# Performance work log

Hardware: AMD Instinct MI355X
Metric: run time of the kernel (lower is better)

The kernel has to match this reference:

```python
import math
import jax, jax.numpy as jnp
import numpy as np

D_MODEL = 1024
N_HEADS = 16
D_K = D_MODEL // N_HEADS


def setup_inputs() -> dict:
    key = jax.random.key(0)
    ks = jax.random.split(key, 12)
    B, L, D = 8, 2048, D_MODEL
    scale = 1.0 / math.sqrt(D)
    inp = {
        "queries": jax.random.normal(ks[0], (B, L, D), jnp.float32),
        "keys": jax.random.normal(ks[1], (B, L, D), jnp.float32),
        "values": jax.random.normal(ks[2], (B, L, D), jnp.float32),
        "Wq": jax.random.normal(ks[3], (D, D), jnp.float32) * scale,
        "bq": jnp.zeros((D,), jnp.float32),
        "Wk": jax.random.normal(ks[4], (D, D), jnp.float32) * scale,
        "bk": jnp.zeros((D,), jnp.float32),
        "Wv": jax.random.normal(ks[5], (D, D), jnp.float32) * scale,
        "bv": jnp.zeros((D,), jnp.float32),
        "Wo": jax.random.normal(ks[6], (D, D), jnp.float32) * scale,
        "bo": jnp.zeros((D,), jnp.float32),
    }
    return inp


def _autocorr_forward(queries, keys, values, Wq, bq, Wk, bk, Wv, bv, Wo, bo):
    B, L, D = queries.shape
    H, dk = N_HEADS, D_K
    # projections (torch Linear: x @ W.T + b), split heads -> [B, L, H, dk]
    q = (queries @ Wq.T + bq).reshape(B, L, H, dk)
    k = (keys @ Wk.T + bk).reshape(B, L, H, dk)
    v = (values @ Wv.T + bv).reshape(B, L, H, dk)

    # FFT cross-correlation along time, averaged over channel dim: [B, L, H]
    qf = jnp.fft.rfft(q, axis=1)
    kf = jnp.fft.rfft(k, axis=1)
    corr = jnp.fft.irfft(qf * jnp.conj(kf), n=L, axis=1).mean(axis=-1)
    corr = corr.transpose(0, 2, 1)  # [B, H, L]

    topk = min(max(1, int(math.log(L))), L)  # top_k=None default
    weights, delays = jax.lax.top_k(corr, topk)  # [B, H, k]
    w = jax.nn.softmax(weights, axis=-1)

    # modulo-shifted gather indices: [B, H, k, L]
    idx = (jnp.arange(L)[None, None, None, :] - delays[..., None]) % L
    v_h = v.transpose(0, 2, 1, 3)  # [B, H, L, dk]
    # gather shifted copies: [B, H, k, L, dk]
    gathered = jnp.take_along_axis(v_h[:, :, None], idx[..., None], axis=3)
    out = (w[..., None, None] * gathered).sum(axis=2)  # [B, H, L, dk]

    out = out.transpose(0, 2, 1, 3).reshape(B, L, D)
    return out @ Wo.T + bo


def reference(queries, keys, values, Wq, bq, Wk, bk, Wv, bv, Wo, bo):
    return _autocorr_forward(queries, keys, values, Wq, bq, Wk, bk, Wv, bv, Wo, bo)
```

## Files before the change

kernel.cpp:

```cpp
#include <hip/hip_runtime.h>
#include <hip/hip_bf16.h>
#include <math.h>

#define B_SZ 8
#define L_SZ 2048
#define D_SZ 1024
#define H_SZ 16
#define DK_SZ 64
#define TOPK 7
#define M_SZ (B_SZ * L_SZ)

typedef __attribute__((ext_vector_type(8))) short short8;
typedef __attribute__((ext_vector_type(4))) float float4v;
typedef unsigned short ushort_t;
typedef unsigned int uint_t;

__device__ __forceinline__ ushort_t f2bf(float x) {
    uint_t u = __float_as_uint(x);
    uint_t r = (u + 0x7fffu + ((u >> 16) & 1u)) >> 16;
    return (ushort_t)r;
}

__device__ __forceinline__ void split8(float4 x, float4 y, short8& hi, short8& lo) {
    float f[8] = {x.x, x.y, x.z, x.w, y.x, y.y, y.z, y.w};
#pragma unroll
    for (int i = 0; i < 8; ++i) {
        uint_t b = __float_as_uint(f[i]);
        hi[i] = (short)(b >> 16);
        float r = f[i] - __uint_as_float(b & 0xffff0000u);
        lo[i] = (short)(__float_as_uint(r) >> 16);
    }
}

__global__ __launch_bounds__(256)
void zero_f32(float* __restrict__ p, int n4) {
    int i = blockIdx.x * 256 + threadIdx.x;
    if (i < n4) ((float4*)p)[i] = make_float4(0.f, 0.f, 0.f, 0.f);
}

__global__ __launch_bounds__(256)
void split_fp32(const float* __restrict__ X, ushort_t* __restrict__ hi,
                ushort_t* __restrict__ lo, int n8) {
    int i = blockIdx.x * 256 + threadIdx.x;
    if (i >= n8) return;
    float4 a = ((const float4*)X)[2 * i];
    float4 b = ((const float4*)X)[2 * i + 1];
    short8 h, l;
    split8(a, b, h, l);
    *(short8*)(hi + (size_t)i * 8) = h;
    *(short8*)(lo + (size_t)i * 8) = l;
}

template <bool BF16OUT>
__global__ __launch_bounds__(256)
void gemm_split_mfma(const float* __restrict__ X, const ushort_t* __restrict__ Whi,
                     const ushort_t* __restrict__ Wlo, const float* __restrict__ bias,
                     void* __restrict__ Yv, int M, int N, int K) {
    __shared__ __align__(16) short Ah[4][128][8];
    __shared__ __align__(16) short Al[4][128][8];
    __shared__ __align__(16) short Bh[4][128][8];
    __shared__ __align__(16) short Bl[4][128][8];

    const int tid = threadIdx.x;
    const int lane = tid & 63;
    const int wave = tid >> 6;
    const int wm = wave >> 1, wn = wave & 1;
    const size_t m0 = (size_t)blockIdx.y * 128;
    const size_t n0 = (size_t)blockIdx.x * 128;

    const int srow = tid >> 1;
    const int g0 = (tid & 1) * 2;
    const int skseg = (tid & 1) * 16;

    const float*    Xp  = X   + (m0 + srow) * K + skseg;
    const ushort_t* Whp = Whi + (n0 + srow) * K + skseg;
    const ushort_t* Wlp = Wlo + (n0 + srow) * K + skseg;

    const int fr = lane & 15;
    const int fg = lane >> 4;

    float4 ax0 = *(const float4*)(Xp + 0);
    float4 ax1 = *(const float4*)(Xp + 4);
    float4 ax2 = *(const float4*)(Xp + 8);
    float4 ax3 = *(const float4*)(Xp + 12);
    short8 bh0 = *(const short8*)(Whp + 0);
    short8 bh1 = *(const short8*)(Whp + 8);
    short8 bl0 = *(const short8*)(Wlp + 0);
    short8 bl1 = *(const short8*)(Wlp + 8);

    float4v acc[4][4];
#pragma unroll
    for (int i = 0; i < 4; ++i)
#pragma unroll
        for (int j = 0; j < 4; ++j) acc[i][j] = (float4v){0.f, 0.f, 0.f, 0.f};

    for (int k0 = 0; k0 < K; k0 += 32) {
        __syncthreads();
        short8 h, l;
        split8(ax0, ax1, h, l);
        *(short8*)&Ah[g0][srow][0] = h;      *(short8*)&Al[g0][srow][0] = l;
        split8(ax2, ax3, h, l);
        *(short8*)&Ah[g0 + 1][srow][0] = h;  *(short8*)&Al[g0 + 1][srow][0] = l;
        *(short8*)&Bh[g0][srow][0] = bh0;    *(short8*)&Bh[g0 + 1][srow][0] = bh1;
        *(short8*)&Bl[g0][srow][0] = bl0;    *(short8*)&Bl[g0 + 1][srow][0] = bl1;
        __syncthreads();

        if (k0 + 32 < K) {
            ax0 = *(const float4*)(Xp + k0 + 32);
            ax1 = *(const float4*)(Xp + k0 + 36);
            ax2 = *(const float4*)(Xp + k0 + 40);
            ax3 = *(const float4*)(Xp + k0 + 44);
            bh0 = *(const short8*)(Whp + k0 + 32);
            bh1 = *(const short8*)(Whp + k0 + 40);
            bl0 = *(const short8*)(Wlp + k0 + 32);
            bl1 = *(const short8*)(Wlp + k0 + 40);
        }

        short8 afh[4], afl[4], bfh[4], bfl[4];
#pragma unroll
        for (int i = 0; i < 4; ++i) {
            const int r = wm * 64 + i * 16 + fr;
            afh[i] = *(const short8*)&Ah[fg][r][0];
            afl[i] = *(const short8*)&Al[fg][r][0];
        }
#pragma unroll
        for (int j = 0; j < 4; ++j) {
            const int r = wn * 64 + j * 16 + fr;
            bfh[j] = *(const short8*)&Bh[fg][r][0];
            bfl[j] = *(const short8*)&Bl[fg][r][0];
        }
#pragma unroll
        for (int i = 0; i < 4; ++i)
#pragma unroll
            for (int j = 0; j < 4; ++j) {
                acc[i][j] = __builtin_amdgcn_mfma_f32_16x16x32_bf16(afh[i], bfh[j], acc[i][j], 0, 0, 0);
                acc[i][j] = __builtin_amdgcn_mfma_f32_16x16x32_bf16(afh[i], bfl[j], acc[i][j], 0, 0, 0);
                acc[i][j] = __builtin_amdgcn_mfma_f32_16x16x32_bf16(afl[i], bfh[j], acc[i][j], 0, 0, 0);
            }
    }

    const int en = fr;
    const int emb = (lane >> 4) * 4;
#pragma unroll
    for (int j = 0; j < 4; ++j) {
        const size_t col = n0 + wn * 64 + j * 16 + en;
        const float bv = bias[col];
#pragma unroll
        for (int i = 0; i < 4; ++i) {
#pragma unroll
            for (int r = 0; r < 4; ++r) {
                const size_t row = m0 + wm * 64 + i * 16 + emb + r;
                const float o = acc[i][j][r] + bv;
                if (BF16OUT) ((ushort_t*)Yv)[row * N + col] = f2bf(o);
                else         ((float*)Yv)[row * N + col] = o;
            }
        }
    }
}

__global__ __launch_bounds__(256)
void corr_mfma(const ushort_t* __restrict__ Qb, const ushort_t* __restrict__ Kb,
               float* __restrict__ corr) {
    const int wave = threadIdx.x >> 6;
    const int lane = threadIdx.x & 63;
    const int bh = blockIdx.x;
    const int jq = blockIdx.y;
    const int b = bh >> 4, h = bh & 15;
    const int jbase = jq * 32 + wave * 8;
    const int lrow = lane & 15;
    const int kgrp = (lane >> 4) * 8;

    const size_t slice = (size_t)b * L_SZ * D_SZ + (size_t)h * DK_SZ;
    const ushort_t* Qp = Qb + slice + kgrp;
    const ushort_t* Kp = Kb + slice + kgrp;

    float4v acc[8];
#pragma unroll
    for (int i = 0; i < 8; ++i) acc[i] = (float4v){0.f, 0.f, 0.f, 0.f};

    short8 Wa[8], Wb[8];
#pragma unroll
    for (int i = 0; i < 8; ++i) {
        const size_t tq = (size_t)((((jbase + i) & 127) << 4) + lrow) * D_SZ;
        Wa[i] = *(const short8*)(Qp + tq);
        Wb[i] = *(const short8*)(Qp + tq + 32);
    }
    short8 kb0 = *(const short8*)(Kp + (size_t)lrow * D_SZ);
    short8 kb1 = *(const short8*)(Kp + (size_t)lrow * D_SZ + 32);

    for (int s8 = 0; s8 < 128; s8 += 8) {
#pragma unroll
        for (int u = 0; u < 8; ++u) {
            const int s0 = s8 + u;
            const size_t sn = (size_t)((((s0 + 1) & 127) << 4) + lrow) * D_SZ;
            short8 nk0 = *(const short8*)(Kp + sn);
            short8 nk1 = *(const short8*)(Kp + sn + 32);

            acc[0] = __builtin_amdgcn_mfma_f32_16x16x32_bf16(Wa[u], kb0, acc[0], 0, 0, 0);
            acc[0] = __builtin_amdgcn_mfma_f32_16x16x32_bf16(Wb[u], kb1, acc[0], 0, 0, 0);
            {
                const size_t tq = (size_t)((((s0 + 8 + jbase) & 127) << 4) + lrow) * D_SZ;
                Wa[u] = *(const short8*)(Qp + tq);
                Wb[u] = *(const short8*)(Qp + tq + 32);
            }
#pragma unroll
            for (int jj = 1; jj < 8; ++jj) {
                acc[jj] = __builtin_amdgcn_mfma_f32_16x16x32_bf16(Wa[(u + jj) & 7], kb0, acc[jj], 0, 0, 0);
                acc[jj] = __builtin_amdgcn_mfma_f32_16x16x32_bf16(Wb[(u + jj) & 7], kb1, acc[jj], 0, 0, 0);
            }
            kb0 = nk0; kb1 = nk1;
        }
    }

    const int n = lane & 15;
    const int mb = (lane >> 4) * 4;
    float* cb = corr + (size_t)bh * L_SZ;
#pragma unroll
    for (int jj = 0; jj < 8; ++jj) {
        const int j16 = (jbase + jj) << 4;
#pragma unroll
        for (int r = 0; r < 4; ++r) {
            const int d = (j16 + mb + r - n) & (L_SZ - 1);
            atomicAdd(cb + d, acc[jj][r] * (1.0f / 64.0f));
        }
    }
}

__global__ __launch_bounds__(256)
void topk_softmax(const float* __restrict__ corr, float* __restrict__ w,
                  int* __restrict__ delays) {
    __shared__ float cv[L_SZ];
    __shared__ float rv[256];
    __shared__ int   ri[256];
    __shared__ float topv[TOPK];
    __shared__ int   topi[TOPK];
    const int bh = blockIdx.x, tid = threadIdx.x;

    for (int i = tid; i < L_SZ; i += 256) cv[i] = corr[(size_t)bh * L_SZ + i];
    __syncthreads();

    for (int it = 0; it < TOPK; ++it) {
        float best = -INFINITY; int bi = 0;
        for (int i = tid; i < L_SZ; i += 256) {
            float x = cv[i];
            if (x > best) { best = x; bi = i; }
        }
        rv[tid] = best; ri[tid] = bi;
        __syncthreads();
        for (int stride = 128; stride > 0; stride >>= 1) {
            if (tid < stride) {
                float ov = rv[tid + stride]; int oi = ri[tid + stride];
                if (ov > rv[tid] || (ov == rv[tid] && oi < ri[tid])) {
                    rv[tid] = ov; ri[tid] = oi;
                }
            }
            __syncthreads();
        }
        if (tid == 0) {
            topv[it] = rv[0]; topi[it] = ri[0];
            cv[ri[0]] = -INFINITY;
        }
        __syncthreads();
    }

    if (tid == 0) {
        float mx = topv[0];
        float e[TOPK], s = 0.f;
#pragma unroll
        for (int i = 0; i < TOPK; ++i) { e[i] = expf(topv[i] - mx); s += e[i]; }
        const float inv = 1.0f / s;
#pragma unroll
        for (int i = 0; i < TOPK; ++i) {
            w[bh * TOPK + i] = e[i] * inv;
            delays[bh * TOPK + i] = topi[i];
        }
    }
}

__global__ __launch_bounds__(256)
void gather_combine(const float* __restrict__ V, const float* __restrict__ w,
                    const int* __restrict__ delays, float* __restrict__ mid) {
    const size_t g = (size_t)blockIdx.x * 256 + threadIdx.x;
    const int c4 = (int)(g & 255);
    const int t  = (int)((g >> 8) & (L_SZ - 1));
    const int b  = (int)(g >> 19);
    const int h  = c4 >> 4;
    const int bh = b * H_SZ + h;
    const size_t colbase = (size_t)b * L_SZ * D_SZ + (size_t)c4 * 4;

    float4 acc = {0.f, 0.f, 0.f, 0.f};
#pragma unroll
    for (int i = 0; i < TOPK; ++i) {
        const float wi = w[bh * TOPK + i];
        const int   di = delays[bh * TOPK + i];
        const int   ts = (t - di) & (L_SZ - 1);
        float4 v4 = *(const float4*)(V + colbase + (size_t)ts * D_SZ);
        acc.x += wi * v4.x; acc.y += wi * v4.y;
        acc.z += wi * v4.z; acc.w += wi * v4.w;
    }
    *(float4*)(mid + (size_t)b * L_SZ * D_SZ + (size_t)t * D_SZ + c4 * 4) = acc;
}

extern "C" void kernel_launch(void* const* d_in, const int* in_sizes, int n_in,
                              void* d_out, int out_size, void* d_ws, size_t ws_size,
                              hipStream_t stream) {
    const float* queries = (const float*)d_in[0];
    const float* keys    = (const float*)d_in[1];
    const float* values  = (const float*)d_in[2];
    const float* Wq = (const float*)d_in[3];
    const float* bq = (const float*)d_in[4];
    const float* Wk = (const float*)d_in[5];
    const float* bk = (const float*)d_in[6];
    const float* Wv = (const float*)d_in[7];
    const float* bv = (const float*)d_in[8];
    const float* Wo = (const float*)d_in[9];
    const float* bo = (const float*)d_in[10];

    const size_t NE = (size_t)M_SZ * D_SZ;
    ushort_t* Qb16 = (ushort_t*)d_ws;
    ushort_t* Kb16 = Qb16 + NE;
    float* Vb   = (float*)(Kb16 + NE);
    float* corr = Vb + NE;
    float* wbuf = corr + (size_t)B_SZ * H_SZ * L_SZ;
    int*   dbuf = (int*)(wbuf + B_SZ * H_SZ * TOPK);
    ushort_t* WH = (ushort_t*)(dbuf + B_SZ * H_SZ * TOPK);
    ushort_t* WL = WH + (size_t)D_SZ * D_SZ;
    float* mid  = (float*)d_ws;

    dim3 ggemm(D_SZ / 128, M_SZ / 128);
    const int wn8 = D_SZ * D_SZ / 8;

    split_fp32<<<(wn8 + 255) / 256, 256, 0, stream>>>(Wq, WH, WL, wn8);
    gemm_split_mfma<true><<<ggemm, 256, 0, stream>>>(queries, WH, WL, bq, Qb16, M_SZ, D_SZ, D_SZ);
    split_fp32<<<(wn8 + 255) / 256, 256, 0, stream>>>(Wk, WH, WL, wn8);
    gemm_split_mfma<true><<<ggemm, 256, 0, stream>>>(keys, WH, WL, bk, Kb16, M_SZ, D_SZ, D_SZ);
    split_fp32<<<(wn8 + 255) / 256, 256, 0, stream>>>(Wv, WH, WL, wn8);
    gemm_split_mfma<false><<<ggemm, 256, 0, stream>>>(values, WH, WL, bv, Vb, M_SZ, D_SZ, D_SZ);

    zero_f32<<<(B_SZ * H_SZ * L_SZ / 4 + 255) / 256, 256, 0, stream>>>(
        corr, B_SZ * H_SZ * L_SZ / 4);

    corr_mfma<<<dim3(B_SZ * H_SZ, 4), 256, 0, stream>>>(Qb16, Kb16, corr);

    topk_softmax<<<B_SZ * H_SZ, 256, 0, stream>>>(corr, wbuf, dbuf);

    gather_combine<<<(M_SZ * 256) / 256, 256, 0, stream>>>(Vb, wbuf, dbuf, mid);

    split_fp32<<<(wn8 + 255) / 256, 256, 0, stream>>>(Wo, WH, WL, wn8);
    gemm_split_mfma<false><<<ggemm, 256, 0, stream>>>(mid, WH, WL, bo, (float*)d_out, M_SZ, D_SZ, D_SZ);
}
```

Before: 871.0 us.

## Stage Q and K tiles through swizzled LDS ring buffers in corr kernel

The correlation kernel now streams Q and K tiles into shared memory with direct global-to-LDS loads into ring buffers: a 28-slot Q ring shared by the block's waves and a 4-slot K ring. Two waves issue Q loads and two issue K loads each step, and every wave reads MFMA operands from XOR-swizzled LDS. Before, each wave loaded the same K rows and overlapping Q rows from global memory itself. The aim is to share loads across the block's waves and cut redundant global traffic, at the cost of a block barrier and a vmcnt wait every iteration plus higher LDS use, which may lower occupancy.

Measured after the change: 816.7 us. 1.07x faster.

```diff
diff --git a/kernel.cpp b/kernel.cpp
--- a/kernel.cpp
+++ b/kernel.cpp
@@ -30,6 +30,12 @@
         float r = f[i] - __uint_as_float(b & 0xffff0000u);
         lo[i] = (short)(__float_as_uint(r) >> 16);
     }
+}
+
+__device__ __forceinline__ void gl_lds16(const ushort_t* g, ushort_t* l) {
+    __builtin_amdgcn_global_load_lds(
+        (const __attribute__((address_space(1))) unsigned int*)g,
+        (__attribute__((address_space(3))) unsigned int*)l, 16, 0, 0);
 }
 
 __global__ __launch_bounds__(256)
@@ -161,47 +167,96 @@
 __global__ __launch_bounds__(256)
 void corr_mfma(const ushort_t* __restrict__ Qb, const ushort_t* __restrict__ Kb,
                float* __restrict__ corr) {
-    const int wave = threadIdx.x >> 6;
-    const int lane = threadIdx.x & 63;
+    __shared__ __align__(16) ushort_t Qlds[28 * 1024];
+    __shared__ __align__(16) ushort_t Klds[4 * 1024];
+
+    const int tid  = threadIdx.x;
+    const int wave = tid >> 6;
+    const int lane = tid & 63;
     const int bh = blockIdx.x;
     const int jq = blockIdx.y;
     const int b = bh >> 4, h = bh & 15;
-    const int jbase = jq * 32 + wave * 8;
-    const int lrow = lane & 15;
-    const int kgrp = (lane >> 4) * 8;
+    const int b0 = jq * 32;
+    const int jbase = b0 + wave * 8;
+    const int rr = lane & 15;
+    const int cq = lane >> 4;
+    const int s7 = rr & 7;
 
     const size_t slice = (size_t)b * L_SZ * D_SZ + (size_t)h * DK_SZ;
-    const ushort_t* Qp = Qb + slice + kgrp;
-    const ushort_t* Kp = Kb + slice + kgrp;
+    const ushort_t* Qs = Qb + slice;
+    const ushort_t* Ks = Kb + slice;
+    const ushort_t* Qp = Qs + cq * 8;
+
+    const int st  = tid & 127;
+    const int sr  = st >> 3;
+    const int sc  = (st & 7) ^ (sr & 7);
+    const int whalf = (wave & 1) * 512;
+
+    const int roff0 = rr * 64 + ((cq ^ s7) * 8);
+    const int roff1 = roff0 ^ 32;
 
     float4v acc[8];
 #pragma unroll
     for (int i = 0; i < 8; ++i) acc[i] = (float4v){0.f, 0.f, 0.f, 0.f};
 
+    if (wave < 2) {
+        for (int i = 0; i < 26; ++i) {
+            const int qt = (b0 + 8 + i) & 127;
+            gl_lds16(Qs + (size_t)(qt * 16 + sr) * 1024 + sc * 8,
+                     &Qlds[i * 1024 + whalf]);
+        }
+    } else {
+        for (int i = 0; i < 3; ++i) {
+            gl_lds16(Ks + (size_t)(i * 16 + sr) * 1024 + sc * 8,
+                     &Klds[i * 1024 + whalf]);
+        }
+    }
+
     short8 Wa[8], Wb[8];
 #pragma unroll
     for (int i = 0; i < 8; ++i) {
-        const size_t tq = (size_t)((((jbase + i) & 127) << 4) + lrow) * D_SZ;
+        const size_t tq = (size_t)((((jbase + i) & 127) << 4) + rr) * D_SZ;
         Wa[i] = *(const short8*)(Qp + tq);
         Wb[i] = *(const short8*)(Qp + tq + 32);
     }
-    short8 kb0 = *(const short8*)(Kp + (size_t)lrow * D_SZ);
-    short8 kb1 = *(const short8*)(Kp + (size_t)lrow * D_SZ + 32);
+
+    asm volatile("s_waitcnt vmcnt(0)" ::: "memory");
+    __builtin_amdgcn_s_barrier();
+    asm volatile("" ::: "memory");
+
+    short8 kb0 = *(const short8*)&Klds[roff0];
+    short8 kb1 = *(const short8*)&Klds[roff1];
+
+    int qsr = wave * 8;
+    int qsw = 26;
 
     for (int s8 = 0; s8 < 128; s8 += 8) {
 #pragma unroll
         for (int u = 0; u < 8; ++u) {
             const int s0 = s8 + u;
-            const size_t sn = (size_t)((((s0 + 1) & 127) << 4) + lrow) * D_SZ;
-            short8 nk0 = *(const short8*)(Kp + sn);
-            short8 nk1 = *(const short8*)(Kp + sn + 32);
+            if (wave < 2) {
+                const int qt = (b0 + 34 + s0) & 127;
+                gl_lds16(Qs + (size_t)(qt * 16 + sr) * 1024 + sc * 8,
+                         &Qlds[qsw * 1024 + whalf]);
+            } else {
+                const int kt = (s0 + 3) & 127;
+                gl_lds16(Ks + (size_t)(kt * 16 + sr) * 1024 + sc * 8,
+                         &Klds[((s0 + 3) & 3) * 1024 + whalf]);
+            }
+            asm volatile("s_waitcnt vmcnt(2)" ::: "memory");
+            __builtin_amdgcn_s_barrier();
+            asm volatile("" ::: "memory");
+
+            const int kslot = ((s0 + 1) & 3) * 1024;
+            short8 nk0 = *(const short8*)&Klds[kslot + roff0];
+            short8 nk1 = *(const short8*)&Klds[kslot + roff1];
 
             acc[0] = __builtin_amdgcn_mfma_f32_16x16x32_bf16(Wa[u], kb0, acc[0], 0, 0, 0);
             acc[0] = __builtin_amdgcn_mfma_f32_16x16x32_bf16(Wb[u], kb1, acc[0], 0, 0, 0);
             {
-                const size_t tq = (size_t)((((s0 + 8 + jbase) & 127) << 4) + lrow) * D_SZ;
-                Wa[u] = *(const short8*)(Qp + tq);
-                Wb[u] = *(const short8*)(Qp + tq + 32);
+                const int qbse = qsr * 1024;
+                Wa[u] = *(const short8*)&Qlds[qbse + roff0];
+                Wb[u] = *(const short8*)&Qlds[qbse + roff1];
             }
 #pragma unroll
             for (int jj = 1; jj < 8; ++jj) {
@@ -209,6 +264,8 @@
                 acc[jj] = __builtin_amdgcn_mfma_f32_16x16x32_bf16(Wb[(u + jj) & 7], kb1, acc[jj], 0, 0, 0);
             }
             kb0 = nk0; kb1 = nk1;
+            qsr = (qsr + 1 == 28) ? 0 : qsr + 1;
+            qsw = (qsw + 1 == 28) ? 0 : qsw + 1;
         }
     }
 
```
